# Kernel optimization log

Measured on AMD Instinct MI355X. Metric: run time of the kernel, lower is better.

Reference implementation:

```python
import jax, jax.numpy as jnp
import numpy as np

DIM = 96
EPS = 1e-5

def setup_inputs() -> dict:
    key = jax.random.key(0)
    k1, k2, k3, k4 = jax.random.split(key, 4)
    x = jax.random.normal(k1, (2, DIM, 32, 64, 64), dtype=jnp.float32)
    # LayerNorm(8*dim) params and Linear(8*dim -> 2*dim, bias=False) weight
    gamma = jnp.ones((8 * DIM,), dtype=jnp.float32)
    beta = jnp.zeros((8 * DIM,), dtype=jnp.float32)
    w_red = jax.random.normal(k2, (8 * DIM, 2 * DIM), dtype=jnp.float32) * (1.0 / np.sqrt(8 * DIM))
    return {"x": x, "gamma": gamma, "beta": beta, "w_red": w_red}


def _patch_merge(x, gamma, beta, w_red):
    B, C, D, H, W = x.shape
    # pad trailing spatial dims to even (static shapes -> python ifs are fine)
    if (D % 2) or (H % 2) or (W % 2):
        x = jnp.pad(x, ((0, 0), (0, 0), (0, D % 2), (0, H % 2), (0, W % 2)))
    x = jnp.transpose(x, (0, 2, 3, 4, 1))  # B, D, H, W, C
    # gather the 8 octant sub-lattices and concat on channel
    parts = [x[:, d::2, h::2, w::2, :]
             for d in (0, 1) for h in (0, 1) for w in (0, 1)]
    # torch order: x0..x7 indexed by (d,h,w) bits with d slowest -> matches loop order
    y = jnp.concatenate(parts, axis=-1)  # B, D/2, H/2, W/2, 8C
    # LayerNorm over last dim
    mu = jnp.mean(y, axis=-1, keepdims=True)
    var = jnp.mean(jnp.square(y - mu), axis=-1, keepdims=True)
    y = (y - mu) * jax.lax.rsqrt(var + EPS) * gamma + beta
    # Linear 8C -> 2C, no bias
    y = jnp.einsum('bdhwc,co->bdhwo', y, w_red)
    return jnp.transpose(y, (0, 4, 1, 2, 3))  # B, 2C, D/2, H/2, W/2


def reference(x, gamma, beta, w_red):
    return _patch_merge(x, gamma, beta, w_red)
```

## Files before the change

kernel.cpp:

```cpp
#include <hip/hip_runtime.h>

typedef __attribute__((ext_vector_type(8))) short short8;
typedef __attribute__((ext_vector_type(4))) float float4v;

__device__ __forceinline__ unsigned short f2bf(float f) {
  unsigned int u = __float_as_uint(f);
  u += 0x7fffu + ((u >> 16) & 1u);
  return (unsigned short)(u >> 16);
}
__device__ __forceinline__ float bf2f(unsigned short h) {
  return __uint_as_float(((unsigned int)h) << 16);
}
__device__ __forceinline__ unsigned int pack2bf(float a, float b) {
  return (unsigned int)f2bf(a) | ((unsigned int)f2bf(b) << 16);
}

__global__ __launch_bounds__(256)
void prep_kernel(const float* __restrict__ w_red, const float* __restrict__ gamma,
                 const float* __restrict__ beta, unsigned short* __restrict__ w_frag,
                 float* __restrict__ colsum, float* __restrict__ bias) {
  const int n = blockIdx.x;
  const int t = threadIdx.x;
  const int ntile = n >> 4, lrow = n & 15;
  float cs = 0.f, bs = 0.f;
#pragma unroll
  for (int j = 0; j < 3; ++j) {
    int kp = j * 256 + t;
    int ko = (kp & 7) * 96 + (kp >> 3);
    float w = w_red[(size_t)ko * 192 + n];
    unsigned short v = f2bf(gamma[ko] * w);
    int kc = kp >> 5, r = kp & 31, lq = r >> 3, e = r & 7;
    w_frag[(size_t)((ntile * 24 + kc) * 64 + lq * 16 + lrow) * 8 + e] = v;
    cs += bf2f(v);
    bs += beta[ko] * w;
  }
#pragma unroll
  for (int off = 1; off < 64; off <<= 1) {
    cs += __shfl_xor(cs, off, 64);
    bs += __shfl_xor(bs, off, 64);
  }
  __shared__ float red[2][4];
  const int wave = t >> 6;
  if ((t & 63) == 0) { red[0][wave] = cs; red[1][wave] = bs; }
  __syncthreads();
  if (t == 0) {
    colsum[n] = red[0][0] + red[0][1] + red[0][2] + red[0][3];
    bias[n]   = red[1][0] + red[1][1] + red[1][2] + red[1][3];
  }
}

__global__ __launch_bounds__(256, 4)
void pm_kernel(const float* __restrict__ x, const unsigned short* __restrict__ w_frag,
               const float* __restrict__ colsum, const float* __restrict__ bias,
               float* __restrict__ out) {
  __shared__ __align__(16) float F[4096];
  __shared__ __align__(16) unsigned short Yb[2048];
  __shared__ float4 part4[4][8];
  __shared__ float smu[16], srs[16];

  const int tid = threadIdx.x;
  const int bid = blockIdx.x;
  const int b  = bid >> 10;
  const int dz = (bid >> 6) & 15;
  const int hy = (bid >> 1) & 31;
  const int wh = bid & 1;

  const float* xb = x + (size_t)b * 12582912u + (size_t)dz * 8192u
                      + (size_t)hy * 128u + wh * 32;
  const int r0 = tid >> 3;
  const int c0 = r0 >> 2;
  const int di = (r0 >> 1) & 1;
  const int hi = r0 & 1;
  const int w0 = (tid & 7) << 2;
  const float* xp = xb + (size_t)c0 * 131072u + di * 4096 + hi * 64 + w0;

  const int lane = tid & 63;
  const int wave = tid >> 6;
  const int lrow = lane & 15;
  const int lq   = lane >> 4;

  char* ybase = (char*)Yb;
  const int wx0 = (tid & 7) << 1;
  const int k00 = c0 * 8 + di * 4 + hi * 2;
  const int b0off = (wx0 * 128 + k00 * 2) ^ ((wx0 & 7) << 4);
  const int b1off = ((wx0 + 1) * 128 + k00 * 2) ^ (((wx0 + 1) & 7) << 4);
  const int ra0 = (lrow * 128 + lq * 16) ^ ((lrow & 7) << 4);
  const int ra1 = (lrow * 128 + 64 + lq * 16) ^ ((lrow & 7) << 4);
  const int fth = wave * 256 + lane * 4;
  const int fwv = wave * 256;

  const unsigned short* wb0 = w_frag + (size_t)(wave * 3 + 0) * 12288u + lane * 8;
  const unsigned short* wb1 = w_frag + (size_t)(wave * 3 + 1) * 12288u + lane * 8;
  const unsigned short* wb2 = w_frag + (size_t)(wave * 3 + 2) * 12288u + lane * 8;

  short8 bA[6], bB[6];
  float4v acc[3];
#pragma unroll
  for (int j = 0; j < 3; ++j)
#pragma unroll
    for (int r = 0; r < 4; ++r) acc[j][r] = 0.f;
  float sum0 = 0.f, sq0 = 0.f, sum1 = 0.f, sq1 = 0.f;

#define DMA(IT, SL)                                                            \
  __builtin_amdgcn_global_load_lds(                                            \
      (const __attribute__((address_space(1))) unsigned int*)(xp + (size_t)(IT) * 1048576u), \
      (__attribute__((address_space(3))) unsigned int*)&F[(SL) * 1024 + fwv], 16, 0, 0)

#define LOADB(BN, ITB)                                                         \
  do {                                                                         \
    const unsigned short* kp0 = wb0 + (ITB) * 1024;                            \
    BN[0] = *(const short8*)(kp0);                                             \
    BN[1] = *(const short8*)(kp0 + 512);                                       \
    const unsigned short* kp1 = wb1 + (ITB) * 1024;                            \
    BN[2] = *(const short8*)(kp1);                                             \
    BN[3] = *(const short8*)(kp1 + 512);                                       \
    const unsigned short* kp2 = wb2 + (ITB) * 1024;                            \
    BN[4] = *(const short8*)(kp2);                                             \
    BN[5] = *(const short8*)(kp2 + 512);                                       \
  } while (0)

#define PACK(SLP, PN)                                                          \
  do {                                                                         \
    float4 vv = *(const float4*)&F[(SLP) * 1024 + fth];                        \
    *(unsigned int*)(ybase + (PN) * 2048 + b0off) = pack2bf(vv.x, vv.y);       \
    *(unsigned int*)(ybase + (PN) * 2048 + b1off) = pack2bf(vv.z, vv.w);       \
    sum0 += vv.x + vv.y;  sq0 += vv.x * vv.x + vv.y * vv.y;                    \
    sum1 += vv.z + vv.w;  sq1 += vv.z * vv.z + vv.w * vv.w;                    \
  } while (0)

#define PHASE(IT, PC, PN, BC, BN, SLI, SLP)                                    \
  do {                                                                         \
    asm volatile("s_waitcnt lgkmcnt(0)" ::: "memory");                         \
    __builtin_amdgcn_s_barrier();                                              \
    { int itb = (IT) + 1 <= 11 ? (IT) + 1 : 11; LOADB(BN, itb); }              \
    __builtin_amdgcn_sched_barrier(0);                                         \
    { int itn = (IT) + 3 <= 11 ? (IT) + 3 : 11; DMA(itn, SLI); }               \
    __builtin_amdgcn_sched_barrier(0);                                         \
    asm volatile("s_waitcnt vmcnt(8)" ::: "memory");                           \
    __builtin_amdgcn_sched_barrier(0);                                         \
    if ((IT) < 11) PACK(SLP, PN);                                              \
    { short8 a0 = *(const short8*)(ybase + (PC) * 2048 + ra0);                 \
      short8 a1 = *(const short8*)(ybase + (PC) * 2048 + ra1);                 \
      acc[0] = __builtin_amdgcn_mfma_f32_16x16x32_bf16(a0, BC[0], acc[0], 0, 0, 0); \
      acc[0] = __builtin_amdgcn_mfma_f32_16x16x32_bf16(a1, BC[1], acc[0], 0, 0, 0); \
      acc[1] = __builtin_amdgcn_mfma_f32_16x16x32_bf16(a0, BC[2], acc[1], 0, 0, 0); \
      acc[1] = __builtin_amdgcn_mfma_f32_16x16x32_bf16(a1, BC[3], acc[1], 0, 0, 0); \
      acc[2] = __builtin_amdgcn_mfma_f32_16x16x32_bf16(a0, BC[4], acc[2], 0, 0, 0); \
      acc[2] = __builtin_amdgcn_mfma_f32_16x16x32_bf16(a1, BC[5], acc[2], 0, 0, 0); } \
  } while (0)

  DMA(0, 0);
  __builtin_amdgcn_sched_barrier(0);
  DMA(1, 1);
  __builtin_amdgcn_sched_barrier(0);
  LOADB(bA, 0);
  __builtin_amdgcn_sched_barrier(0);
  DMA(2, 2);
  __builtin_amdgcn_sched_barrier(0);
  asm volatile("s_waitcnt vmcnt(8)" ::: "memory");
  __builtin_amdgcn_sched_barrier(0);
  PACK(0, 0);

#pragma unroll
  for (int it4 = 0; it4 < 12; it4 += 4) {
    PHASE(it4 + 0, 0, 1, bA, bB, 3, 1);
    PHASE(it4 + 1, 1, 0, bB, bA, 0, 2);
    PHASE(it4 + 2, 0, 1, bA, bB, 1, 3);
    PHASE(it4 + 3, 1, 0, bB, bA, 2, 0);
  }
#undef PHASE
#undef PACK
#undef LOADB
#undef DMA

#pragma unroll
  for (int off = 8; off < 64; off <<= 1) {
    sum0 += __shfl_xor(sum0, off, 64);  sq0 += __shfl_xor(sq0, off, 64);
    sum1 += __shfl_xor(sum1, off, 64);  sq1 += __shfl_xor(sq1, off, 64);
  }
  if (lane < 8) part4[wave][lane] = make_float4(sum0, sq0, sum1, sq1);
  __syncthreads();

  if (tid < 16) {
    int l = tid >> 1, odd = tid & 1;
    float s = 0.f, q = 0.f;
#pragma unroll
    for (int w = 0; w < 4; ++w) {
      float4 p = part4[w][l];
      s += odd ? p.z : p.x;
      q += odd ? p.w : p.y;
    }
    float mu  = s * (1.f / 768.f);
    float var = q * (1.f / 768.f) - mu * mu;
    smu[tid] = mu;
    srs[tid] = rsqrtf(var + 1e-5f);
  }
  __syncthreads();

  float4 mu4 = *(const float4*)&smu[lq * 4];
  float4 rs4 = *(const float4*)&srs[lq * 4];
  float* ob = out + (size_t)b * 3145728u + (size_t)dz * 1024u
                  + (size_t)hy * 32u + wh * 16 + lq * 4;
#pragma unroll
  for (int j = 0; j < 3; ++j) {
    int n = (wave * 3 + j) * 16 + lrow;
    float cs = colsum[n], bi = bias[n];
    float4 vv;
    vv.x = rs4.x * (acc[j][0] - mu4.x * cs) + bi;
    vv.y = rs4.y * (acc[j][1] - mu4.y * cs) + bi;
    vv.z = rs4.z * (acc[j][2] - mu4.z * cs) + bi;
    vv.w = rs4.w * (acc[j][3] - mu4.w * cs) + bi;
    *(float4*)(ob + (size_t)n * 16384u) = vv;
  }
}

extern "C" void kernel_launch(void* const* d_in, const int* in_sizes, int n_in,
                              void* d_out, int out_size, void* d_ws, size_t ws_size,
                              hipStream_t stream) {
  const float* x     = (const float*)d_in[0];
  const float* gamma = (const float*)d_in[1];
  const float* beta  = (const float*)d_in[2];
  const float* w_red = (const float*)d_in[3];
  float* out = (float*)d_out;

  unsigned short* w_frag = (unsigned short*)d_ws;
  float* colsum = (float*)((char*)d_ws + 294912);
  float* bias   = colsum + 192;

  prep_kernel<<<dim3(192), dim3(256), 0, stream>>>(w_red, gamma, beta, w_frag, colsum, bias);
  pm_kernel<<<dim3(2048), dim3(256), 0, stream>>>(x, w_frag, colsum, bias, out);
}
```

Before: 192.9 us.

## Double per-block M tile to 32 rows to reuse weight fragments

Each block now handles a full 32-wide W row (two 16-row M tiles) instead of half, so every loaded weight B fragment feeds twice as many MFMAs, which halves the global weight traffic per output. LDS staging buffers, DMA per phase and statistics reductions are doubled to match, and the grid shrinks to 1024 blocks with launch bounds lowered to 3 waves-per-EU. The cost is more LDS and registers per block and fewer blocks, which reduces occupancy and latency hiding for this memory-bound kernel.

Measured after the change: 185.3 us. 3.9% less time.

```diff
diff --git a/kernel.cpp b/kernel.cpp
--- a/kernel.cpp
+++ b/kernel.cpp
@@ -49,62 +49,73 @@
   }
 }
 
-__global__ __launch_bounds__(256, 4)
+__global__ __launch_bounds__(256, 3)
 void pm_kernel(const float* __restrict__ x, const unsigned short* __restrict__ w_frag,
                const float* __restrict__ colsum, const float* __restrict__ bias,
                float* __restrict__ out) {
-  __shared__ __align__(16) float F[4096];
-  __shared__ __align__(16) unsigned short Yb[2048];
-  __shared__ float4 part4[4][8];
-  __shared__ float smu[16], srs[16];
+  __shared__ __align__(16) float F[8192];
+  __shared__ __align__(16) unsigned short Yb[4096];
+  __shared__ float4 part4[4][16];
+  __shared__ float smu[32], srs[32];
 
   const int tid = threadIdx.x;
   const int bid = blockIdx.x;
-  const int b  = bid >> 10;
-  const int dz = (bid >> 6) & 15;
-  const int hy = (bid >> 1) & 31;
-  const int wh = bid & 1;
+  const int b  = bid >> 9;
+  const int dz = (bid >> 5) & 15;
+  const int hy = bid & 31;
 
   const float* xb = x + (size_t)b * 12582912u + (size_t)dz * 8192u
-                      + (size_t)hy * 128u + wh * 32;
-  const int r0 = tid >> 3;
-  const int c0 = r0 >> 2;
-  const int di = (r0 >> 1) & 1;
-  const int hi = r0 & 1;
-  const int w0 = (tid & 7) << 2;
-  const float* xp = xb + (size_t)c0 * 131072u + di * 4096 + hi * 64 + w0;
+                      + (size_t)hy * 128u;
 
   const int lane = tid & 63;
   const int wave = tid >> 6;
   const int lrow = lane & 15;
   const int lq   = lane >> 4;
 
+  const int di = (lane >> 5) & 1;
+  const int hi = (lane >> 4) & 1;
+  const float* xp0 = xb + (size_t)(2 * wave) * 131072u + di * 4096 + hi * 64
+                        + ((lane & 15) << 2);
+  const float* xp1 = xp0 + 131072u;
+
   char* ybase = (char*)Yb;
-  const int wx0 = (tid & 7) << 1;
-  const int k00 = c0 * 8 + di * 4 + hi * 2;
-  const int b0off = (wx0 * 128 + k00 * 2) ^ ((wx0 & 7) << 4);
-  const int b1off = ((wx0 + 1) * 128 + k00 * 2) ^ (((wx0 + 1) & 7) << 4);
-  const int ra0 = (lrow * 128 + lq * 16) ^ ((lrow & 7) << 4);
-  const int ra1 = (lrow * 128 + 64 + lq * 16) ^ ((lrow & 7) << 4);
-  const int fth = wave * 256 + lane * 4;
-  const int fwv = wave * 256;
+  const int wx0 = (lane & 15) << 1;
+  const int k0d0 = wave * 16 + di * 4 + hi * 2;
+  const int k0d1 = k0d0 + 8;
+  const int b00 = (wx0 * 128 + k0d0 * 2) ^ ((wx0 & 7) << 4);
+  const int b01 = ((wx0 + 1) * 128 + k0d0 * 2) ^ (((wx0 + 1) & 7) << 4);
+  const int b10 = (wx0 * 128 + k0d1 * 2) ^ ((wx0 & 7) << 4);
+  const int b11 = ((wx0 + 1) * 128 + k0d1 * 2) ^ (((wx0 + 1) & 7) << 4);
+  const int ra00 = (lrow * 128 + lq * 16) ^ ((lrow & 7) << 4);
+  const int ra01 = (lrow * 128 + 64 + lq * 16) ^ ((lrow & 7) << 4);
+  const int ra10 = ((16 + lrow) * 128 + lq * 16) ^ ((lrow & 7) << 4);
+  const int ra11 = ((16 + lrow) * 128 + 64 + lq * 16) ^ ((lrow & 7) << 4);
+  const int fth = wave * 512 + lane * 4;
+  const int fwv = wave * 512;
 
   const unsigned short* wb0 = w_frag + (size_t)(wave * 3 + 0) * 12288u + lane * 8;
   const unsigned short* wb1 = w_frag + (size_t)(wave * 3 + 1) * 12288u + lane * 8;
   const unsigned short* wb2 = w_frag + (size_t)(wave * 3 + 2) * 12288u + lane * 8;
 
   short8 bA[6], bB[6];
-  float4v acc[3];
-#pragma unroll
-  for (int j = 0; j < 3; ++j)
-#pragma unroll
-    for (int r = 0; r < 4; ++r) acc[j][r] = 0.f;
+  float4v acc[2][3];
+#pragma unroll
+  for (int mt = 0; mt < 2; ++mt)
+#pragma unroll
+    for (int j = 0; j < 3; ++j)
+#pragma unroll
+      for (int r = 0; r < 4; ++r) acc[mt][j][r] = 0.f;
   float sum0 = 0.f, sq0 = 0.f, sum1 = 0.f, sq1 = 0.f;
 
-#define DMA(IT, SL)                                                            \
-  __builtin_amdgcn_global_load_lds(                                            \
-      (const __attribute__((address_space(1))) unsigned int*)(xp + (size_t)(IT) * 1048576u), \
-      (__attribute__((address_space(3))) unsigned int*)&F[(SL) * 1024 + fwv], 16, 0, 0)
+#define DMA2(IT, SL)                                                           \
+  do {                                                                         \
+    __builtin_amdgcn_global_load_lds(                                          \
+        (const __attribute__((address_space(1))) unsigned int*)(xp0 + (size_t)(IT) * 1048576u), \
+        (__attribute__((address_space(3))) unsigned int*)&F[(SL) * 2048 + fwv], 16, 0, 0); \
+    __builtin_amdgcn_global_load_lds(                                          \
+        (const __attribute__((address_space(1))) unsigned int*)(xp1 + (size_t)(IT) * 1048576u), \
+        (__attribute__((address_space(3))) unsigned int*)&F[(SL) * 2048 + fwv + 256], 16, 0, 0); \
+  } while (0)
 
 #define LOADB(BN, ITB)                                                         \
   do {                                                                         \
@@ -121,11 +132,16 @@
 
 #define PACK(SLP, PN)                                                          \
   do {                                                                         \
-    float4 vv = *(const float4*)&F[(SLP) * 1024 + fth];                        \
-    *(unsigned int*)(ybase + (PN) * 2048 + b0off) = pack2bf(vv.x, vv.y);       \
-    *(unsigned int*)(ybase + (PN) * 2048 + b1off) = pack2bf(vv.z, vv.w);       \
-    sum0 += vv.x + vv.y;  sq0 += vv.x * vv.x + vv.y * vv.y;                    \
-    sum1 += vv.z + vv.w;  sq1 += vv.z * vv.z + vv.w * vv.w;                    \
+    float4 v0 = *(const float4*)&F[(SLP) * 2048 + fth];                        \
+    float4 v1 = *(const float4*)&F[(SLP) * 2048 + fth + 256];                  \
+    *(unsigned int*)(ybase + (PN) * 4096 + b00) = pack2bf(v0.x, v0.y);         \
+    *(unsigned int*)(ybase + (PN) * 4096 + b01) = pack2bf(v0.z, v0.w);         \
+    *(unsigned int*)(ybase + (PN) * 4096 + b10) = pack2bf(v1.x, v1.y);         \
+    *(unsigned int*)(ybase + (PN) * 4096 + b11) = pack2bf(v1.z, v1.w);         \
+    sum0 += v0.x + v0.y + v1.x + v1.y;                                         \
+    sq0  += v0.x * v0.x + v0.y * v0.y + v1.x * v1.x + v1.y * v1.y;             \
+    sum1 += v0.z + v0.w + v1.z + v1.w;                                         \
+    sq1  += v0.z * v0.z + v0.w * v0.w + v1.z * v1.z + v1.w * v1.w;             \
   } while (0)
 
 #define PHASE(IT, PC, PN, BC, BN, SLI, SLP)                                    \
@@ -134,30 +150,38 @@
     __builtin_amdgcn_s_barrier();                                              \
     { int itb = (IT) + 1 <= 11 ? (IT) + 1 : 11; LOADB(BN, itb); }              \
     __builtin_amdgcn_sched_barrier(0);                                         \
-    { int itn = (IT) + 3 <= 11 ? (IT) + 3 : 11; DMA(itn, SLI); }               \
+    { int itn = (IT) + 3 <= 11 ? (IT) + 3 : 11; DMA2(itn, SLI); }              \
     __builtin_amdgcn_sched_barrier(0);                                         \
-    asm volatile("s_waitcnt vmcnt(8)" ::: "memory");                           \
+    asm volatile("s_waitcnt vmcnt(10)" ::: "memory");                          \
     __builtin_amdgcn_sched_barrier(0);                                         \
     if ((IT) < 11) PACK(SLP, PN);                                              \
-    { short8 a0 = *(const short8*)(ybase + (PC) * 2048 + ra0);                 \
-      short8 a1 = *(const short8*)(ybase + (PC) * 2048 + ra1);                 \
-      acc[0] = __builtin_amdgcn_mfma_f32_16x16x32_bf16(a0, BC[0], acc[0], 0, 0, 0); \
-      acc[0] = __builtin_amdgcn_mfma_f32_16x16x32_bf16(a1, BC[1], acc[0], 0, 0, 0); \
-      acc[1] = __builtin_amdgcn_mfma_f32_16x16x32_bf16(a0, BC[2], acc[1], 0, 0, 0); \
-      acc[1] = __builtin_amdgcn_mfma_f32_16x16x32_bf16(a1, BC[3], acc[1], 0, 0, 0); \
-      acc[2] = __builtin_amdgcn_mfma_f32_16x16x32_bf16(a0, BC[4], acc[2], 0, 0, 0); \
-      acc[2] = __builtin_amdgcn_mfma_f32_16x16x32_bf16(a1, BC[5], acc[2], 0, 0, 0); } \
-  } while (0)
-
-  DMA(0, 0);
-  __builtin_amdgcn_sched_barrier(0);
-  DMA(1, 1);
+    { short8 a00 = *(const short8*)(ybase + (PC) * 4096 + ra00);               \
+      short8 a01 = *(const short8*)(ybase + (PC) * 4096 + ra01);               \
+      short8 a10 = *(const short8*)(ybase + (PC) * 4096 + ra10);               \
+      short8 a11 = *(const short8*)(ybase + (PC) * 4096 + ra11);               \
+      acc[0][0] = __builtin_amdgcn_mfma_f32_16x16x32_bf16(a00, BC[0], acc[0][0], 0, 0, 0); \
+      acc[0][0] = __builtin_amdgcn_mfma_f32_16x16x32_bf16(a01, BC[1], acc[0][0], 0, 0, 0); \
+      acc[1][0] = __builtin_amdgcn_mfma_f32_16x16x32_bf16(a10, BC[0], acc[1][0], 0, 0, 0); \
+      acc[1][0] = __builtin_amdgcn_mfma_f32_16x16x32_bf16(a11, BC[1], acc[1][0], 0, 0, 0); \
+      acc[0][1] = __builtin_amdgcn_mfma_f32_16x16x32_bf16(a00, BC[2], acc[0][1], 0, 0, 0); \
+      acc[0][1] = __builtin_amdgcn_mfma_f32_16x16x32_bf16(a01, BC[3], acc[0][1], 0, 0, 0); \
+      acc[1][1] = __builtin_amdgcn_mfma_f32_16x16x32_bf16(a10, BC[2], acc[1][1], 0, 0, 0); \
+      acc[1][1] = __builtin_amdgcn_mfma_f32_16x16x32_bf16(a11, BC[3], acc[1][1], 0, 0, 0); \
+      acc[0][2] = __builtin_amdgcn_mfma_f32_16x16x32_bf16(a00, BC[4], acc[0][2], 0, 0, 0); \
+      acc[0][2] = __builtin_amdgcn_mfma_f32_16x16x32_bf16(a01, BC[5], acc[0][2], 0, 0, 0); \
+      acc[1][2] = __builtin_amdgcn_mfma_f32_16x16x32_bf16(a10, BC[4], acc[1][2], 0, 0, 0); \
+      acc[1][2] = __builtin_amdgcn_mfma_f32_16x16x32_bf16(a11, BC[5], acc[1][2], 0, 0, 0); } \
+  } while (0)
+
+  DMA2(0, 0);
+  __builtin_amdgcn_sched_barrier(0);
+  DMA2(1, 1);
   __builtin_amdgcn_sched_barrier(0);
   LOADB(bA, 0);
   __builtin_amdgcn_sched_barrier(0);
-  DMA(2, 2);
-  __builtin_amdgcn_sched_barrier(0);
-  asm volatile("s_waitcnt vmcnt(8)" ::: "memory");
+  DMA2(2, 2);
+  __builtin_amdgcn_sched_barrier(0);
+  asm volatile("s_waitcnt vmcnt(10)" ::: "memory");
   __builtin_amdgcn_sched_barrier(0);
   PACK(0, 0);
 
@@ -171,22 +195,22 @@
 #undef PHASE
 #undef PACK
 #undef LOADB
-#undef DMA
-
-#pragma unroll
-  for (int off = 8; off < 64; off <<= 1) {
+#undef DMA2
+
+#pragma unroll
+  for (int off = 16; off < 64; off <<= 1) {
     sum0 += __shfl_xor(sum0, off, 64);  sq0 += __shfl_xor(sq0, off, 64);
     sum1 += __shfl_xor(sum1, off, 64);  sq1 += __shfl_xor(sq1, off, 64);
   }
-  if (lane < 8) part4[wave][lane] = make_float4(sum0, sq0, sum1, sq1);
+  if (lane < 16) part4[wave][lane] = make_float4(sum0, sq0, sum1, sq1);
   __syncthreads();
 
-  if (tid < 16) {
-    int l = tid >> 1, odd = tid & 1;
+  if (tid < 32) {
+    int sp = tid >> 1, odd = tid & 1;
     float s = 0.f, q = 0.f;
 #pragma unroll
     for (int w = 0; w < 4; ++w) {
-      float4 p = part4[w][l];
+      float4 p = part4[w][sp];
       s += odd ? p.z : p.x;
       q += odd ? p.w : p.y;
     }
@@ -197,20 +221,26 @@
   }
   __syncthreads();
 
-  float4 mu4 = *(const float4*)&smu[lq * 4];
-  float4 rs4 = *(const float4*)&srs[lq * 4];
-  float* ob = out + (size_t)b * 3145728u + (size_t)dz * 1024u
-                  + (size_t)hy * 32u + wh * 16 + lq * 4;
+  float4 mu4a = *(const float4*)&smu[lq * 4];
+  float4 rs4a = *(const float4*)&srs[lq * 4];
+  float4 mu4b = *(const float4*)&smu[16 + lq * 4];
+  float4 rs4b = *(const float4*)&srs[16 + lq * 4];
+  float* ob = out + (size_t)b * 3145728u + (size_t)dz * 1024u + (size_t)hy * 32u;
 #pragma unroll
   for (int j = 0; j < 3; ++j) {
     int n = (wave * 3 + j) * 16 + lrow;
     float cs = colsum[n], bi = bias[n];
     float4 vv;
-    vv.x = rs4.x * (acc[j][0] - mu4.x * cs) + bi;
-    vv.y = rs4.y * (acc[j][1] - mu4.y * cs) + bi;
-    vv.z = rs4.z * (acc[j][2] - mu4.z * cs) + bi;
-    vv.w = rs4.w * (acc[j][3] - mu4.w * cs) + bi;
-    *(float4*)(ob + (size_t)n * 16384u) = vv;
+    vv.x = rs4a.x * (acc[0][j][0] - mu4a.x * cs) + bi;
+    vv.y = rs4a.y * (acc[0][j][1] - mu4a.y * cs) + bi;
+    vv.z = rs4a.z * (acc[0][j][2] - mu4a.z * cs) + bi;
+    vv.w = rs4a.w * (acc[0][j][3] - mu4a.w * cs) + bi;
+    *(float4*)(ob + (size_t)n * 16384u + lq * 4) = vv;
+    vv.x = rs4b.x * (acc[1][j][0] - mu4b.x * cs) + bi;
+    vv.y = rs4b.y * (acc[1][j][1] - mu4b.y * cs) + bi;
+    vv.z = rs4b.z * (acc[1][j][2] - mu4b.z * cs) + bi;
+    vv.w = rs4b.w * (acc[1][j][3] - mu4b.w * cs) + bi;
+    *(float4*)(ob + (size_t)n * 16384u + 16 + lq * 4) = vv;
   }
 }
 
@@ -228,5 +258,5 @@
   float* bias   = colsum + 192;
 
   prep_kernel<<<dim3(192), dim3(256), 0, stream>>>(w_red, gamma, beta, w_frag, colsum, bias);
-  pm_kernel<<<dim3(2048), dim3(256), 0, stream>>>(x, w_frag, colsum, bias, out);
-}
+  pm_kernel<<<dim3(1024), dim3(256), 0, stream>>>(x, w_frag, colsum, bias, out);
+}
```
